# Performance work log

Measured on AMD Instinct MI355X. Metric: run time of the kernel, lower is better.

## Reference

```python
import jax, jax.numpy as jnp
import numpy as np

N = 200_000       # nodes
K = 16            # fixed in-degree
E = N * K         # edges
G = 4_000         # graphs (50 nodes each)
F_IN, H1, H2, OUT = 25, 16, 8, 2
EPS = 1e-5        # PyG std aggregator epsilon


def setup_inputs() -> dict:
    key = jax.random.key(0)
    ks = jax.random.split(key, 10)
    x = jax.random.normal(ks[0], (N, F_IN), jnp.float32)
    src = jax.random.randint(ks[1], (E,), 0, N)
    dst = jnp.repeat(jnp.arange(N), K)          # every node gets K incoming edges
    edge_index = jnp.stack([src, dst]).astype(jnp.int32)
    batch = jnp.repeat(jnp.arange(G), N // G).astype(jnp.int32)

    def lin(k, o, i):
        s = 1.0 / np.sqrt(i)
        kw, kb = jax.random.split(k)
        return (jax.random.uniform(kw, (o, i), jnp.float32, -s, s),
                jax.random.uniform(kb, (o,), jnp.float32, -s, s))

    w1_pre, b1_pre = lin(ks[2], F_IN, 2 * F_IN)
    w1_post, b1_post = lin(ks[3], H1, 12 * F_IN)
    w1_lin, b1_lin = lin(ks[4], H1, H1)
    w2_pre, b2_pre = lin(ks[5], H1, 2 * H1)
    w2_post, b2_post = lin(ks[6], H2, 12 * H1)
    w2_lin, b2_lin = lin(ks[7], H2, H2)
    fc_w, fc_b = lin(ks[8], OUT, H2)
    return dict(x=x, edge_index=edge_index, batch=batch,
                w1_pre=w1_pre, b1_pre=b1_pre, w1_post=w1_post, b1_post=b1_post,
                w1_lin=w1_lin, b1_lin=b1_lin,
                w2_pre=w2_pre, b2_pre=b2_pre, w2_post=w2_post, b2_post=b2_post,
                w2_lin=w2_lin, b2_lin=b2_lin, fc_w=fc_w, fc_b=fc_b)


def pna_conv(x, edge_index, wp, bp, wo, bo, wl, bl):
    src, dst = edge_index[0], edge_index[1]
    # message: pre-MLP on concat([x_i, x_j])  (x_i = target, x_j = source)
    m = jnp.concatenate([x[dst], x[src]], axis=-1) @ wp.T + bp  # [E, F]
    cnt = jax.ops.segment_sum(jnp.ones((m.shape[0],), m.dtype), dst, N)  # in-degree
    cnt_c = jnp.maximum(cnt, 1.0)[:, None]
    mean = jax.ops.segment_sum(m, dst, N) / cnt_c
    mean2 = jax.ops.segment_sum(m * m, dst, N) / cnt_c
    std = jnp.sqrt(jax.nn.relu(mean2 - mean * mean) + EPS)
    has = cnt[:, None] > 0
    mn = jnp.where(has, jax.ops.segment_min(m, dst, N), 0.0)
    mx = jnp.where(has, jax.ops.segment_max(m, dst, N), 0.0)
    agg = jnp.concatenate([mean, mn, mx, std], axis=-1)  # [N, 4F]
    # degree scalers (identity / amplification / attenuation)
    logd = jnp.log(jnp.maximum(cnt, 1.0) + 1.0)[:, None]
    avg_log = jnp.mean(jnp.log(cnt + 1.0))
    out = jnp.concatenate([agg, agg * (logd / avg_log), agg * (avg_log / logd)], axis=-1)
    out = out @ wo.T + bo   # post MLP
    return out @ wl.T + bl  # final lin


def reference(x, edge_index, batch,
              w1_pre, b1_pre, w1_post, b1_post, w1_lin, b1_lin,
              w2_pre, b2_pre, w2_post, b2_post, w2_lin, b2_lin,
              fc_w, fc_b):
    h = jax.nn.relu(pna_conv(x, edge_index, w1_pre, b1_pre, w1_post, b1_post, w1_lin, b1_lin))
    # dropout is identity in eval mode
    h = jax.nn.relu(pna_conv(h, edge_index, w2_pre, b2_pre, w2_post, b2_post, w2_lin, b2_lin))
    pooled = jax.ops.segment_sum(h, batch, G)  # global_add_pool -> [G, H2]
    logits = pooled @ fc_w.T + fc_b
    return jax.nn.log_softmax(logits, axis=1)
```

## Files before the change

### kernel.cpp

```cpp
#include <hip/hip_runtime.h>
#include <math.h>

#define N_NODES 200000
#define K_DEG 16
#define G_GRAPHS 4000
#define F_IN 25
#define EPSV 1e-5f

__device__ inline unsigned short f2bf(float f) {
    unsigned int u = __float_as_uint(f);
    u += 0x7fff + ((u >> 16) & 1);
    return (unsigned short)(u >> 16);
}
__device__ inline float bf2f(unsigned short h) {
    return __uint_as_float(((unsigned int)h) << 16);
}

__global__ void prep(const float* __restrict__ w1_pre, const float* __restrict__ b1_pre,
                     const float* __restrict__ w1_post, const float* __restrict__ b1_post,
                     const float* __restrict__ w1_lin, const float* __restrict__ b1_lin,
                     const float* __restrict__ w2_pre, const float* __restrict__ b2_pre,
                     const float* __restrict__ w2_post, const float* __restrict__ b2_post,
                     const float* __restrict__ w2_lin, const float* __restrict__ b2_lin,
                     float* __restrict__ C1ext, float* __restrict__ bvp1, float* __restrict__ P1,
                     float* __restrict__ C2p, float* __restrict__ bvp2, float* __restrict__ P2) {
    __shared__ float wp[4800];
    __shared__ float wl[256];
    __shared__ float mm[1600];
    __shared__ float aa[400];
    int tid = threadIdx.x;
    for (int i = tid; i < 4800; i += 256) wp[i] = w1_post[i];
    if (tid < 256) wl[tid] = w1_lin[tid];
    __syncthreads();
    for (int i = tid; i < 1600; i += 256) {
        int o = i / 100, j = i % 100;
        float s = 0.f;
        for (int h = 0; h < 16; ++h)
            s += wl[o * 16 + h] * (wp[h * 300 + j] + wp[h * 300 + 100 + j] + wp[h * 300 + 200 + j]);
        mm[i] = s;
    }
    __syncthreads();
    for (int i = tid; i < 400; i += 256) {
        int o = i / 25, f = i % 25;
        aa[i] = mm[o * 100 + f] + mm[o * 100 + 25 + f] + mm[o * 100 + 50 + f];
    }
    __syncthreads();
    for (int i = tid; i < 1728; i += 256) {
        int o = i / 108, c = i % 108;
        int st = c / 26, f = c % 26;
        C1ext[i] = (c < 104 && f < 25) ? mm[o * 100 + st * 25 + f] : 0.f;
    }
    for (int i = tid; i < 400; i += 256) {
        int o = i / 25, k = i % 25;
        float s = 0.f;
        for (int f = 0; f < 25; ++f) s += aa[o * 25 + f] * w1_pre[f * 50 + k];
        P1[i] = s;
    }
    if (tid < 16) {
        float s = b1_lin[tid];
        for (int h = 0; h < 16; ++h) s += wl[tid * 16 + h] * b1_post[h];
        for (int f = 0; f < 25; ++f) s += aa[tid * 25 + f] * b1_pre[f];
        bvp1[tid] = s;
    }
    __syncthreads();
    for (int i = tid; i < 1536; i += 256) wp[i] = w2_post[i];
    if (tid < 64) wl[tid] = w2_lin[tid];
    __syncthreads();
    for (int i = tid; i < 512; i += 256) {
        int o = i / 64, j = i % 64;
        float s = 0.f;
        for (int h = 0; h < 8; ++h)
            s += wl[o * 8 + h] * (wp[h * 192 + j] + wp[h * 192 + 64 + j] + wp[h * 192 + 128 + j]);
        mm[i] = s;
    }
    __syncthreads();
    if (tid < 128) {
        int o = tid / 16, f = tid % 16;
        aa[tid] = mm[o * 64 + f] + mm[o * 64 + 16 + f] + mm[o * 64 + 32 + f];
    }
    __syncthreads();
    for (int i = tid; i < 544; i += 256) {
        int o = i / 68, c = i % 68;
        C2p[i] = (c < 64) ? mm[o * 64 + c] : 0.f;
    }
    if (tid < 128) {
        int o = tid / 16, k = tid % 16;
        float s = 0.f;
        for (int f = 0; f < 16; ++f) s += aa[o * 16 + f] * w2_pre[f * 32 + k];
        P2[tid] = s;
    }
    if (tid < 8) {
        float s = b2_lin[tid];
        for (int h = 0; h < 8; ++h) s += wl[tid * 8 + h] * b2_post[h];
        for (int f = 0; f < 16; ++f) s += aa[tid * 16 + f] * b2_pre[f];
        bvp2[tid] = s;
    }
}

__global__ void __launch_bounds__(256) pre1(const float* __restrict__ x,
                                            const float* __restrict__ w1_pre,
                                            const float* __restrict__ P1,
                                            unsigned int* __restrict__ c1b_dw,
                                            float* __restrict__ d1) {
    __shared__ float xs[256 * 25];
    __shared__ float wls[25 * 25];
    __shared__ float pls[16 * 25];
    __shared__ unsigned int otile[256 * 17];
    int tid = threadIdx.x;
    int base = blockIdx.x * 256;
    for (int i = tid; i < 6400; i += 256) {
        int g = base * 25 + i;
        xs[i] = (g < N_NODES * F_IN) ? x[g] : 0.f;
    }
    for (int i = tid; i < 625; i += 256) {
        int f = i / 25, k = i % 25;
        wls[i] = w1_pre[f * 50 + 25 + k];
    }
    for (int i = tid; i < 400; i += 256) pls[i] = P1[i];
    __syncthreads();

    float xr[25];
#pragma unroll
    for (int k = 0; k < 25; ++k) xr[k] = xs[tid * 25 + k];

    unsigned int pk[16];
#pragma unroll
    for (int j = 0; j < 16; ++j) pk[j] = 0;
#pragma unroll
    for (int f = 0; f < 25; ++f) {
        float s = 0.f;
#pragma unroll
        for (int k = 0; k < 25; ++k) s += wls[f * 25 + k] * xr[k];
        unsigned int b = f2bf(s);
        pk[f >> 1] |= (f & 1) ? (b << 16) : b;
    }
#pragma unroll
    for (int j = 0; j < 16; ++j) otile[tid * 17 + j] = pk[j];
    __syncthreads();
    for (int i = tid; i < 4096; i += 256) {
        int g = base * 16 + i;
        if (g < N_NODES * 16) c1b_dw[g] = otile[(i >> 4) * 17 + (i & 15)];
    }
    __syncthreads();

    float* ftile = (float*)otile;
#pragma unroll
    for (int o = 0; o < 16; ++o) {
        float s = 0.f;
#pragma unroll
        for (int k = 0; k < 25; ++k) s += pls[o * 25 + k] * xr[k];
        ftile[tid * 17 + o] = s;
    }
    __syncthreads();
    for (int i = tid; i < 4096; i += 256) {
        int g = base * 16 + i;
        if (g < N_NODES * 16) d1[g] = ftile[(i >> 4) * 17 + (i & 15)];
    }
}

__global__ void __launch_bounds__(256) agg1(const unsigned int* __restrict__ c1u,
                                            const int* __restrict__ src,
                                            const float* __restrict__ d1,
                                            const float* __restrict__ C1ext,
                                            const float* __restrict__ bvp1,
                                            const float* __restrict__ w2_pre,
                                            const float* __restrict__ P2,
                                            unsigned short* __restrict__ c2b,
                                            float* __restrict__ d2) {
    __shared__ float cs[16 * 108];
    __shared__ float aggs[16 * 108];
    __shared__ float h1s[16 * 17];
    __shared__ float ws2[16 * 17];
    __shared__ float p2s[8 * 17];
    __shared__ float bvs[16];
    __shared__ int idxs[256];
    int tid = threadIdx.x;
    for (int i = tid; i < 1728; i += 256) cs[i] = C1ext[i];
    {
        int f = tid >> 4, k = tid & 15;
        ws2[f * 17 + k] = w2_pre[f * 32 + 16 + k];
    }
    if (tid < 128) p2s[(tid >> 4) * 17 + (tid & 15)] = P2[tid];
    if (tid < 16) bvs[tid] = bvp1[tid];
    idxs[tid] = src[blockIdx.x * 256 + tid];
    __syncthreads();

    int g = tid >> 4;
    int L = tid & 15;
    {
        int id[K_DEG];
#pragma unroll
        for (int e = 0; e < K_DEG; ++e) id[e] = idxs[g * 16 + e];
        unsigned int v[K_DEG];
#pragma unroll
        for (int e = 0; e < K_DEG; ++e) v[e] = c1u[id[e] * 16 + L];
        float s0 = 0.f, q0 = 0.f, n0 = 1e30f, x0 = -1e30f;
        float s1 = 0.f, q1 = 0.f, n1 = 1e30f, x1 = -1e30f;
#pragma unroll
        for (int e = 0; e < K_DEG; ++e) {
            float a = bf2f((unsigned short)(v[e] & 0xffff));
            float b = bf2f((unsigned short)(v[e] >> 16));
            s0 += a; q0 += a * a; n0 = fminf(n0, a); x0 = fmaxf(x0, a);
            s1 += b; q1 += b * b; n1 = fminf(n1, b); x1 = fmaxf(x1, b);
        }
        float me0 = s0 * (1.f / 16.f), me1 = s1 * (1.f / 16.f);
        float sd0 = sqrtf(fmaxf(q0 * (1.f / 16.f) - me0 * me0, 0.f) + EPSV);
        float sd1 = sqrtf(fmaxf(q1 * (1.f / 16.f) - me1 * me1, 0.f) + EPSV);
        if (L < 13) {
            float* r = aggs + g * 108 + 2 * L;
            *(float2*)(r)      = make_float2(me0, me1);
            *(float2*)(r + 26) = make_float2(n0, n1);
            *(float2*)(r + 52) = make_float2(x0, x1);
            *(float2*)(r + 78) = make_float2(sd0, sd1);
        } else if (L == 13) {
            *(float4*)(aggs + g * 108 + 104) = make_float4(0.f, 0.f, 0.f, 0.f);
        }
    }
    __syncthreads();

    {
        int nl = tid >> 4, o = tid & 15;
        int nn = blockIdx.x * 16 + nl;
        float s = bvs[o] + d1[nn * 16 + o];
        const float4* c4 = (const float4*)(cs + o * 108);
        const float4* a4 = (const float4*)(aggs + nl * 108);
#pragma unroll
        for (int j = 0; j < 27; ++j) {
            float4 cv = c4[j], av = a4[j];
            s += cv.x * av.x + cv.y * av.y + cv.z * av.z + cv.w * av.w;
        }
        h1s[nl * 17 + o] = fmaxf(s, 0.f);
    }
    __syncthreads();

    {
        int nl = tid >> 4, f = tid & 15;
        int nn = blockIdx.x * 16 + nl;
        const float* hr = h1s + nl * 17;
        float s = 0.f;
#pragma unroll
        for (int k = 0; k < 16; ++k) s += ws2[f * 17 + k] * hr[k];
        c2b[nn * 16 + f] = f2bf(s);
    }
    if (tid < 128) {
        int nl = tid >> 3, o = tid & 7;
        int nn = blockIdx.x * 16 + nl;
        const float* hr = h1s + nl * 17;
        float s = 0.f;
#pragma unroll
        for (int k = 0; k < 16; ++k) s += p2s[o * 17 + k] * hr[k];
        d2[nn * 8 + o] = s;
    }
}

__global__ void __launch_bounds__(256) agg2(const unsigned int* __restrict__ c2u,
                                            const int* __restrict__ src,
                                            const float* __restrict__ d2,
                                            const float* __restrict__ C2p,
                                            const float* __restrict__ bvp2,
                                            float* __restrict__ h2) {
    __shared__ float cs[8 * 68];
    __shared__ float ag[32 * 68];
    __shared__ float bvs[8];
    __shared__ int idxs[512];
    int tid = threadIdx.x;
    for (int i = tid; i < 544; i += 256) cs[i] = C2p[i];
    if (tid < 8) bvs[tid] = bvp2[tid];
    idxs[tid] = src[blockIdx.x * 512 + tid];
    idxs[tid + 256] = src[blockIdx.x * 512 + 256 + tid];
    __syncthreads();

    int g = tid >> 3;
    int L = tid & 7;
    {
        int id[K_DEG];
#pragma unroll
        for (int e = 0; e < K_DEG; ++e) id[e] = idxs[g * 16 + e];
        unsigned int v[K_DEG];
#pragma unroll
        for (int e = 0; e < K_DEG; ++e) v[e] = c2u[id[e] * 8 + L];
        float s0 = 0.f, q0 = 0.f, n0 = 1e30f, x0 = -1e30f;
        float s1 = 0.f, q1 = 0.f, n1 = 1e30f, x1 = -1e30f;
#pragma unroll
        for (int e = 0; e < K_DEG; ++e) {
            float a = bf2f((unsigned short)(v[e] & 0xffff));
            float b = bf2f((unsigned short)(v[e] >> 16));
            s0 += a; q0 += a * a; n0 = fminf(n0, a); x0 = fmaxf(x0, a);
            s1 += b; q1 += b * b; n1 = fminf(n1, b); x1 = fmaxf(x1, b);
        }
        float me0 = s0 * (1.f / 16.f), me1 = s1 * (1.f / 16.f);
        float sd0 = sqrtf(fmaxf(q0 * (1.f / 16.f) - me0 * me0, 0.f) + EPSV);
        float sd1 = sqrtf(fmaxf(q1 * (1.f / 16.f) - me1 * me1, 0.f) + EPSV);
        float* r = ag + g * 68 + 2 * L;
        *(float2*)(r)      = make_float2(me0, me1);
        *(float2*)(r + 16) = make_float2(n0, n1);
        *(float2*)(r + 32) = make_float2(x0, x1);
        *(float2*)(r + 48) = make_float2(sd0, sd1);
        if (L == 0) *(float4*)(ag + g * 68 + 64) = make_float4(0.f, 0.f, 0.f, 0.f);
    }
    __syncthreads();

    {
        int nl = tid >> 3, o = tid & 7;
        int nn = blockIdx.x * 32 + nl;
        float s = bvs[o] + d2[nn * 8 + o];
        const float4* c4 = (const float4*)(cs + o * 68);
        const float4* a4 = (const float4*)(ag + nl * 68);
#pragma unroll
        for (int j = 0; j < 17; ++j) {
            float4 cv = c4[j], av = a4[j];
            s += cv.x * av.x + cv.y * av.y + cv.z * av.z + cv.w * av.w;
        }
        h2[nn * 8 + o] = fmaxf(s, 0.f);
    }
}

__global__ void pool_fc(const float* __restrict__ h2, const float* __restrict__ fc_w,
                        const float* __restrict__ fc_b, float* __restrict__ out) {
    int wave = threadIdx.x >> 6;
    int lane = threadIdx.x & 63;
    int g = blockIdx.x * 4 + wave;
    float s0 = 0.f, s1 = 0.f;
    if (lane < 50) {
        const float* hr = h2 + (g * 50 + lane) * 8;
        float v[8];
#pragma unroll
        for (int o = 0; o < 8; ++o) v[o] = hr[o];
#pragma unroll
        for (int o = 0; o < 8; ++o) { s0 += fc_w[o] * v[o]; s1 += fc_w[8 + o] * v[o]; }
    }
#pragma unroll
    for (int off = 32; off > 0; off >>= 1) {
        s0 += __shfl_down(s0, off);
        s1 += __shfl_down(s1, off);
    }
    if (lane == 0) {
        float l0 = s0 + fc_b[0], l1 = s1 + fc_b[1];
        float m = fmaxf(l0, l1);
        float lse = m + logf(expf(l0 - m) + expf(l1 - m));
        out[g * 2]     = l0 - lse;
        out[g * 2 + 1] = l1 - lse;
    }
}

extern "C" void kernel_launch(void* const* d_in, const int* in_sizes, int n_in,
                              void* d_out, int out_size, void* d_ws, size_t ws_size,
                              hipStream_t stream) {
    const float* x       = (const float*)d_in[0];
    const int*   eidx    = (const int*)d_in[1];
    const float* w1_pre  = (const float*)d_in[3];
    const float* b1_pre  = (const float*)d_in[4];
    const float* w1_post = (const float*)d_in[5];
    const float* b1_post = (const float*)d_in[6];
    const float* w1_lin  = (const float*)d_in[7];
    const float* b1_lin  = (const float*)d_in[8];
    const float* w2_pre  = (const float*)d_in[9];
    const float* b2_pre  = (const float*)d_in[10];
    const float* w2_post = (const float*)d_in[11];
    const float* b2_post = (const float*)d_in[12];
    const float* w2_lin  = (const float*)d_in[13];
    const float* b2_lin  = (const float*)d_in[14];
    const float* fc_w    = (const float*)d_in[15];
    const float* fc_b    = (const float*)d_in[16];
    float* out = (float*)d_out;
    const int* src = eidx;

    char* ws = (char*)d_ws;
    unsigned int*   c1u = (unsigned int*)ws;
    unsigned short* c2b = (unsigned short*)(ws + 12800000);
    float* d1  = (float*)(ws + 19200000);
    float* d2  = (float*)(ws + 32000000);
    float* h2  = (float*)(ws + 38400000);
    float* C1ext = (float*)(ws + 44800000);
    float* bvp1  = C1ext + 1728;
    float* P1    = bvp1 + 16;
    float* C2p   = P1 + 400;
    float* bvp2  = C2p + 544;
    float* P2    = bvp2 + 8;

    prep<<<1, 256, 0, stream>>>(w1_pre, b1_pre, w1_post, b1_post, w1_lin, b1_lin,
                                w2_pre, b2_pre, w2_post, b2_post, w2_lin, b2_lin,
                                C1ext, bvp1, P1, C2p, bvp2, P2);
    pre1<<<(N_NODES + 255) / 256, 256, 0, stream>>>(x, w1_pre, P1, c1u, d1);
    agg1<<<N_NODES / 16, 256, 0, stream>>>(c1u, src, d1, C1ext, bvp1, w2_pre, P2, c2b, d2);
    agg2<<<N_NODES / 32, 256, 0, stream>>>((const unsigned int*)c2b, src, d2, C2p, bvp2, h2);
    pool_fc<<<G_GRAPHS / 4, 256, 0, stream>>>(h2, fc_w, fc_b, out);
}
```

Before: 241.9 us.

## Fold weight prep into consumer kernels and widen per-thread gather to 4 features

Removes the single-block prep kernel and has pre1, agg1 and agg2 each recompute their folded weight matrices and bias vectors in shared memory at block start. This drops one launch and a serial single-block step, but repeats the small weight-folding work in every block. The aggregation kernels now handle twice as many nodes per block, and each thread gathers uint2 (four bf16 features) per edge instead of one uint32. The goal is fewer, wider gather loads and better amortization of the per-block setup.

```diff
diff --git a/kernel.cpp b/kernel.cpp
--- a/kernel.cpp
+++ b/kernel.cpp
@@ -16,95 +16,18 @@
     return __uint_as_float(((unsigned int)h) << 16);
 }
 
-__global__ void prep(const float* __restrict__ w1_pre, const float* __restrict__ b1_pre,
-                     const float* __restrict__ w1_post, const float* __restrict__ b1_post,
-                     const float* __restrict__ w1_lin, const float* __restrict__ b1_lin,
-                     const float* __restrict__ w2_pre, const float* __restrict__ b2_pre,
-                     const float* __restrict__ w2_post, const float* __restrict__ b2_post,
-                     const float* __restrict__ w2_lin, const float* __restrict__ b2_lin,
-                     float* __restrict__ C1ext, float* __restrict__ bvp1, float* __restrict__ P1,
-                     float* __restrict__ C2p, float* __restrict__ bvp2, float* __restrict__ P2) {
-    __shared__ float wp[4800];
-    __shared__ float wl[256];
-    __shared__ float mm[1600];
-    __shared__ float aa[400];
-    int tid = threadIdx.x;
-    for (int i = tid; i < 4800; i += 256) wp[i] = w1_post[i];
-    if (tid < 256) wl[tid] = w1_lin[tid];
-    __syncthreads();
-    for (int i = tid; i < 1600; i += 256) {
-        int o = i / 100, j = i % 100;
-        float s = 0.f;
-        for (int h = 0; h < 16; ++h)
-            s += wl[o * 16 + h] * (wp[h * 300 + j] + wp[h * 300 + 100 + j] + wp[h * 300 + 200 + j]);
-        mm[i] = s;
-    }
-    __syncthreads();
-    for (int i = tid; i < 400; i += 256) {
-        int o = i / 25, f = i % 25;
-        aa[i] = mm[o * 100 + f] + mm[o * 100 + 25 + f] + mm[o * 100 + 50 + f];
-    }
-    __syncthreads();
-    for (int i = tid; i < 1728; i += 256) {
-        int o = i / 108, c = i % 108;
-        int st = c / 26, f = c % 26;
-        C1ext[i] = (c < 104 && f < 25) ? mm[o * 100 + st * 25 + f] : 0.f;
-    }
-    for (int i = tid; i < 400; i += 256) {
-        int o = i / 25, k = i % 25;
-        float s = 0.f;
-        for (int f = 0; f < 25; ++f) s += aa[o * 25 + f] * w1_pre[f * 50 + k];
-        P1[i] = s;
-    }
-    if (tid < 16) {
-        float s = b1_lin[tid];
-        for (int h = 0; h < 16; ++h) s += wl[tid * 16 + h] * b1_post[h];
-        for (int f = 0; f < 25; ++f) s += aa[tid * 25 + f] * b1_pre[f];
-        bvp1[tid] = s;
-    }
-    __syncthreads();
-    for (int i = tid; i < 1536; i += 256) wp[i] = w2_post[i];
-    if (tid < 64) wl[tid] = w2_lin[tid];
-    __syncthreads();
-    for (int i = tid; i < 512; i += 256) {
-        int o = i / 64, j = i % 64;
-        float s = 0.f;
-        for (int h = 0; h < 8; ++h)
-            s += wl[o * 8 + h] * (wp[h * 192 + j] + wp[h * 192 + 64 + j] + wp[h * 192 + 128 + j]);
-        mm[i] = s;
-    }
-    __syncthreads();
-    if (tid < 128) {
-        int o = tid / 16, f = tid % 16;
-        aa[tid] = mm[o * 64 + f] + mm[o * 64 + 16 + f] + mm[o * 64 + 32 + f];
-    }
-    __syncthreads();
-    for (int i = tid; i < 544; i += 256) {
-        int o = i / 68, c = i % 68;
-        C2p[i] = (c < 64) ? mm[o * 64 + c] : 0.f;
-    }
-    if (tid < 128) {
-        int o = tid / 16, k = tid % 16;
-        float s = 0.f;
-        for (int f = 0; f < 16; ++f) s += aa[o * 16 + f] * w2_pre[f * 32 + k];
-        P2[tid] = s;
-    }
-    if (tid < 8) {
-        float s = b2_lin[tid];
-        for (int h = 0; h < 8; ++h) s += wl[tid * 8 + h] * b2_post[h];
-        for (int f = 0; f < 16; ++f) s += aa[tid * 16 + f] * b2_pre[f];
-        bvp2[tid] = s;
-    }
-}
-
 __global__ void __launch_bounds__(256) pre1(const float* __restrict__ x,
                                             const float* __restrict__ w1_pre,
-                                            const float* __restrict__ P1,
+                                            const float* __restrict__ w1_post,
+                                            const float* __restrict__ w1_lin,
                                             unsigned int* __restrict__ c1b_dw,
                                             float* __restrict__ d1) {
     __shared__ float xs[256 * 25];
     __shared__ float wls[25 * 25];
     __shared__ float pls[16 * 25];
+    __shared__ float u1[16 * 25];
+    __shared__ float a1s[16 * 25];
+    __shared__ float wl[256];
     __shared__ unsigned int otile[256 * 17];
     int tid = threadIdx.x;
     int base = blockIdx.x * 256;
@@ -116,7 +39,29 @@
         int f = i / 25, k = i % 25;
         wls[i] = w1_pre[f * 50 + 25 + k];
     }
-    for (int i = tid; i < 400; i += 256) pls[i] = P1[i];
+    wl[tid] = w1_lin[tid];
+    for (int i = tid; i < 400; i += 256) {
+        int h = i / 25, f = i % 25;
+        const float* wp = w1_post + h * 300 + f;
+        u1[i] = wp[0] + wp[25] + wp[50] + wp[100] + wp[125] + wp[150] +
+                wp[200] + wp[225] + wp[250];
+    }
+    __syncthreads();
+    for (int i = tid; i < 400; i += 256) {
+        int o = i / 25, f = i % 25;
+        float s = 0.f;
+#pragma unroll
+        for (int h = 0; h < 16; ++h) s += wl[o * 16 + h] * u1[h * 25 + f];
+        a1s[i] = s;
+    }
+    __syncthreads();
+    for (int i = tid; i < 400; i += 256) {
+        int o = i / 25, k = i % 25;
+        float s = 0.f;
+#pragma unroll
+        for (int f = 0; f < 25; ++f) s += a1s[o * 25 + f] * w1_pre[f * 50 + k];
+        pls[i] = s;
+    }
     __syncthreads();
 
     float xr[25];
@@ -158,74 +103,149 @@
     }
 }
 
-__global__ void __launch_bounds__(256) agg1(const unsigned int* __restrict__ c1u,
+__global__ void __launch_bounds__(256) agg1(const uint2* __restrict__ c1u2,
                                             const int* __restrict__ src,
                                             const float* __restrict__ d1,
-                                            const float* __restrict__ C1ext,
-                                            const float* __restrict__ bvp1,
+                                            const float* __restrict__ w1_post,
+                                            const float* __restrict__ w1_lin,
+                                            const float* __restrict__ b1_post,
+                                            const float* __restrict__ b1_lin,
+                                            const float* __restrict__ b1_pre,
                                             const float* __restrict__ w2_pre,
-                                            const float* __restrict__ P2,
+                                            const float* __restrict__ w2_post,
+                                            const float* __restrict__ w2_lin,
                                             unsigned short* __restrict__ c2b,
                                             float* __restrict__ d2) {
-    __shared__ float cs[16 * 108];
-    __shared__ float aggs[16 * 108];
-    __shared__ float h1s[16 * 17];
+    __shared__ float cs[16 * 116];
+    __shared__ float aggs[32 * 116];
+    __shared__ float h1s[32 * 17];
     __shared__ float ws2[16 * 17];
     __shared__ float p2s[8 * 17];
     __shared__ float bvs[16];
-    __shared__ int idxs[256];
+    __shared__ float wl1[256];
+    __shared__ float wl2[64];
+    __shared__ int idxs[512];
     int tid = threadIdx.x;
-    for (int i = tid; i < 1728; i += 256) cs[i] = C1ext[i];
+    float* T1  = aggs;
+    float* T2  = aggs + 1600;
+    float* A1f = aggs + 2112;
+    float* A2f = aggs + 2512;
+
+    for (int i = tid; i < 1600; i += 256) {
+        int h = i / 100, j = i % 100;
+        const float* wp = w1_post + h * 300 + j;
+        T1[i] = wp[0] + wp[100] + wp[200];
+    }
+    for (int i = tid; i < 512; i += 256) {
+        int h = i >> 6, j = i & 63;
+        const float* wp = w2_post + h * 192 + j;
+        T2[i] = wp[0] + wp[64] + wp[128];
+    }
+    wl1[tid] = w1_lin[tid];
+    if (tid < 64) wl2[tid] = w2_lin[tid];
+    { int f = tid >> 4, k = tid & 15; ws2[f * 17 + k] = w2_pre[f * 32 + 16 + k]; }
+    __syncthreads();
+    for (int i = tid; i < 1792; i += 256) {
+        int o = i / 112, c = i % 112;
+        int st = c / 28, f = c % 28;
+        float s = 0.f;
+        if (f < 25) {
+            const float* tr = T1 + st * 25 + f;
+#pragma unroll
+            for (int h = 0; h < 16; ++h) s += wl1[o * 16 + h] * tr[h * 100];
+        }
+        cs[o * 116 + c] = s;
+    }
+    __syncthreads();
+    for (int i = tid; i < 400; i += 256) {
+        int o = i / 25, f = i % 25;
+        A1f[i] = cs[o * 116 + f] + cs[o * 116 + 28 + f] + cs[o * 116 + 56 + f];
+    }
+    if (tid < 128) {
+        int o = tid >> 4, f = tid & 15;
+        float s = 0.f;
+#pragma unroll
+        for (int h = 0; h < 8; ++h)
+            s += wl2[o * 8 + h] * (T2[h * 64 + f] + T2[h * 64 + 16 + f] + T2[h * 64 + 32 + f]);
+        A2f[tid] = s;
+    }
+    __syncthreads();
+    if (tid < 128) {
+        int o = tid >> 4, k = tid & 15;
+        float s = 0.f;
+#pragma unroll
+        for (int f = 0; f < 16; ++f) s += A2f[o * 16 + f] * w2_pre[f * 32 + k];
+        p2s[o * 17 + k] = s;
+    }
+    if (tid < 16) {
+        float s = b1_lin[tid];
+#pragma unroll
+        for (int h = 0; h < 16; ++h) s += wl1[tid * 16 + h] * b1_post[h];
+#pragma unroll
+        for (int f = 0; f < 25; ++f) s += A1f[tid * 25 + f] * b1_pre[f];
+        bvs[tid] = s;
+    }
+    idxs[tid] = src[blockIdx.x * 512 + tid];
+    idxs[256 + tid] = src[blockIdx.x * 512 + 256 + tid];
+    __syncthreads();
+
+    int g = tid >> 3, L = tid & 7;
+    float s0 = 0.f, s1 = 0.f, s2 = 0.f, s3 = 0.f;
+    float q0 = 0.f, q1 = 0.f, q2 = 0.f, q3 = 0.f;
+    float n0 = 1e30f, n1 = 1e30f, n2 = 1e30f, n3 = 1e30f;
+    float x0 = -1e30f, x1 = -1e30f, x2 = -1e30f, x3 = -1e30f;
+#pragma unroll
+    for (int b = 0; b < 2; ++b) {
+        int id[8];
+#pragma unroll
+        for (int e = 0; e < 8; ++e) id[e] = idxs[g * 16 + b * 8 + e];
+        uint2 v[8];
+#pragma unroll
+        for (int e = 0; e < 8; ++e) v[e] = c1u2[id[e] * 8 + L];
+#pragma unroll
+        for (int e = 0; e < 8; ++e) {
+            float a = bf2f((unsigned short)(v[e].x & 0xffff));
+            float bb = bf2f((unsigned short)(v[e].x >> 16));
+            float c = bf2f((unsigned short)(v[e].y & 0xffff));
+            float dd = bf2f((unsigned short)(v[e].y >> 16));
+            s0 += a;  q0 += a * a;   n0 = fminf(n0, a);  x0 = fmaxf(x0, a);
+            s1 += bb; q1 += bb * bb; n1 = fminf(n1, bb); x1 = fmaxf(x1, bb);
+            s2 += c;  q2 += c * c;   n2 = fminf(n2, c);  x2 = fmaxf(x2, c);
+            s3 += dd; q3 += dd * dd; n3 = fminf(n3, dd); x3 = fmaxf(x3, dd);
+        }
+    }
+    float me0 = s0 * (1.f / 16.f), me1 = s1 * (1.f / 16.f);
+    float me2 = s2 * (1.f / 16.f), me3 = s3 * (1.f / 16.f);
+    float sd0 = sqrtf(fmaxf(q0 * (1.f / 16.f) - me0 * me0, 0.f) + EPSV);
+    float sd1 = sqrtf(fmaxf(q1 * (1.f / 16.f) - me1 * me1, 0.f) + EPSV);
+    float sd2 = sqrtf(fmaxf(q2 * (1.f / 16.f) - me2 * me2, 0.f) + EPSV);
+    float sd3 = sqrtf(fmaxf(q3 * (1.f / 16.f) - me3 * me3, 0.f) + EPSV);
     {
-        int f = tid >> 4, k = tid & 15;
-        ws2[f * 17 + k] = w2_pre[f * 32 + 16 + k];
-    }
-    if (tid < 128) p2s[(tid >> 4) * 17 + (tid & 15)] = P2[tid];
-    if (tid < 16) bvs[tid] = bvp1[tid];
-    idxs[tid] = src[blockIdx.x * 256 + tid];
-    __syncthreads();
-
-    int g = tid >> 4;
-    int L = tid & 15;
-    {
-        int id[K_DEG];
-#pragma unroll
-        for (int e = 0; e < K_DEG; ++e) id[e] = idxs[g * 16 + e];
-        unsigned int v[K_DEG];
-#pragma unroll
-        for (int e = 0; e < K_DEG; ++e) v[e] = c1u[id[e] * 16 + L];
-        float s0 = 0.f, q0 = 0.f, n0 = 1e30f, x0 = -1e30f;
-        float s1 = 0.f, q1 = 0.f, n1 = 1e30f, x1 = -1e30f;
-#pragma unroll
-        for (int e = 0; e < K_DEG; ++e) {
-            float a = bf2f((unsigned short)(v[e] & 0xffff));
-            float b = bf2f((unsigned short)(v[e] >> 16));
-            s0 += a; q0 += a * a; n0 = fminf(n0, a); x0 = fmaxf(x0, a);
-            s1 += b; q1 += b * b; n1 = fminf(n1, b); x1 = fmaxf(x1, b);
-        }
-        float me0 = s0 * (1.f / 16.f), me1 = s1 * (1.f / 16.f);
-        float sd0 = sqrtf(fmaxf(q0 * (1.f / 16.f) - me0 * me0, 0.f) + EPSV);
-        float sd1 = sqrtf(fmaxf(q1 * (1.f / 16.f) - me1 * me1, 0.f) + EPSV);
-        if (L < 13) {
-            float* r = aggs + g * 108 + 2 * L;
-            *(float2*)(r)      = make_float2(me0, me1);
-            *(float2*)(r + 26) = make_float2(n0, n1);
-            *(float2*)(r + 52) = make_float2(x0, x1);
-            *(float2*)(r + 78) = make_float2(sd0, sd1);
-        } else if (L == 13) {
-            *(float4*)(aggs + g * 108 + 104) = make_float4(0.f, 0.f, 0.f, 0.f);
-        }
-    }
-    __syncthreads();
-
-    {
-        int nl = tid >> 4, o = tid & 15;
-        int nn = blockIdx.x * 16 + nl;
+        float* r = aggs + g * 116 + 4 * L;
+        if (L < 6) {
+            *(float4*)(r)      = make_float4(me0, me1, me2, me3);
+            *(float4*)(r + 28) = make_float4(n0, n1, n2, n3);
+            *(float4*)(r + 56) = make_float4(x0, x1, x2, x3);
+            *(float4*)(r + 84) = make_float4(sd0, sd1, sd2, sd3);
+        } else if (L == 6) {
+            *(float4*)(r)      = make_float4(me0, 0.f, 0.f, 0.f);
+            *(float4*)(r + 28) = make_float4(n0, 0.f, 0.f, 0.f);
+            *(float4*)(r + 56) = make_float4(x0, 0.f, 0.f, 0.f);
+            *(float4*)(r + 84) = make_float4(sd0, 0.f, 0.f, 0.f);
+        }
+    }
+    __syncthreads();
+
+#pragma unroll
+    for (int r2 = 0; r2 < 2; ++r2) {
+        int t2 = tid + 256 * r2;
+        int nl = t2 >> 4, o = t2 & 15;
+        int nn = blockIdx.x * 32 + nl;
         float s = bvs[o] + d1[nn * 16 + o];
-        const float4* c4 = (const float4*)(cs + o * 108);
-        const float4* a4 = (const float4*)(aggs + nl * 108);
-#pragma unroll
-        for (int j = 0; j < 27; ++j) {
+        const float4* c4 = (const float4*)(cs + o * 116);
+        const float4* a4 = (const float4*)(aggs + nl * 116);
+#pragma unroll
+        for (int j = 0; j < 28; ++j) {
             float4 cv = c4[j], av = a4[j];
             s += cv.x * av.x + cv.y * av.y + cv.z * av.z + cv.w * av.w;
         }
@@ -233,79 +253,131 @@
     }
     __syncthreads();
 
-    {
-        int nl = tid >> 4, f = tid & 15;
-        int nn = blockIdx.x * 16 + nl;
+#pragma unroll
+    for (int r2 = 0; r2 < 2; ++r2) {
+        int t2 = tid + 256 * r2;
+        int nl = t2 >> 4, f = t2 & 15;
+        int nn = blockIdx.x * 32 + nl;
         const float* hr = h1s + nl * 17;
         float s = 0.f;
 #pragma unroll
         for (int k = 0; k < 16; ++k) s += ws2[f * 17 + k] * hr[k];
         c2b[nn * 16 + f] = f2bf(s);
     }
-    if (tid < 128) {
-        int nl = tid >> 3, o = tid & 7;
-        int nn = blockIdx.x * 16 + nl;
-        const float* hr = h1s + nl * 17;
-        float s = 0.f;
-#pragma unroll
-        for (int k = 0; k < 16; ++k) s += p2s[o * 17 + k] * hr[k];
-        d2[nn * 8 + o] = s;
-    }
-}
-
-__global__ void __launch_bounds__(256) agg2(const unsigned int* __restrict__ c2u,
-                                            const int* __restrict__ src,
-                                            const float* __restrict__ d2,
-                                            const float* __restrict__ C2p,
-                                            const float* __restrict__ bvp2,
-                                            float* __restrict__ h2) {
-    __shared__ float cs[8 * 68];
-    __shared__ float ag[32 * 68];
-    __shared__ float bvs[8];
-    __shared__ int idxs[512];
-    int tid = threadIdx.x;
-    for (int i = tid; i < 544; i += 256) cs[i] = C2p[i];
-    if (tid < 8) bvs[tid] = bvp2[tid];
-    idxs[tid] = src[blockIdx.x * 512 + tid];
-    idxs[tid + 256] = src[blockIdx.x * 512 + 256 + tid];
-    __syncthreads();
-
-    int g = tid >> 3;
-    int L = tid & 7;
-    {
-        int id[K_DEG];
-#pragma unroll
-        for (int e = 0; e < K_DEG; ++e) id[e] = idxs[g * 16 + e];
-        unsigned int v[K_DEG];
-#pragma unroll
-        for (int e = 0; e < K_DEG; ++e) v[e] = c2u[id[e] * 8 + L];
-        float s0 = 0.f, q0 = 0.f, n0 = 1e30f, x0 = -1e30f;
-        float s1 = 0.f, q1 = 0.f, n1 = 1e30f, x1 = -1e30f;
-#pragma unroll
-        for (int e = 0; e < K_DEG; ++e) {
-            float a = bf2f((unsigned short)(v[e] & 0xffff));
-            float b = bf2f((unsigned short)(v[e] >> 16));
-            s0 += a; q0 += a * a; n0 = fminf(n0, a); x0 = fmaxf(x0, a);
-            s1 += b; q1 += b * b; n1 = fminf(n1, b); x1 = fmaxf(x1, b);
-        }
-        float me0 = s0 * (1.f / 16.f), me1 = s1 * (1.f / 16.f);
-        float sd0 = sqrtf(fmaxf(q0 * (1.f / 16.f) - me0 * me0, 0.f) + EPSV);
-        float sd1 = sqrtf(fmaxf(q1 * (1.f / 16.f) - me1 * me1, 0.f) + EPSV);
-        float* r = ag + g * 68 + 2 * L;
-        *(float2*)(r)      = make_float2(me0, me1);
-        *(float2*)(r + 16) = make_float2(n0, n1);
-        *(float2*)(r + 32) = make_float2(x0, x1);
-        *(float2*)(r + 48) = make_float2(sd0, sd1);
-        if (L == 0) *(float4*)(ag + g * 68 + 64) = make_float4(0.f, 0.f, 0.f, 0.f);
-    }
-    __syncthreads();
-
     {
         int nl = tid >> 3, o = tid & 7;
         int nn = blockIdx.x * 32 + nl;
-        float s = bvs[o] + d2[nn * 8 + o];
-        const float4* c4 = (const float4*)(cs + o * 68);
-        const float4* a4 = (const float4*)(ag + nl * 68);
+        const float* hr = h1s + nl * 17;
+        float s = 0.f;
+#pragma unroll
+        for (int k = 0; k < 16; ++k) s += p2s[o * 17 + k] * hr[k];
+        d2[nn * 8 + o] = s;
+    }
+}
+
+__global__ void __launch_bounds__(256) agg2(const uint2* __restrict__ c2u2,
+                                            const int* __restrict__ src,
+                                            const float* __restrict__ d2,
+                                            const float* __restrict__ w2_post,
+                                            const float* __restrict__ w2_lin,
+                                            const float* __restrict__ b2_post,
+                                            const float* __restrict__ b2_lin,
+                                            const float* __restrict__ b2_pre,
+                                            float* __restrict__ h2) {
+    __shared__ float cs2[8 * 68];
+    __shared__ float aggs2[64 * 68];
+    __shared__ float wl2[64];
+    __shared__ float bvs2[8];
+    __shared__ int idxs[1024];
+    int tid = threadIdx.x;
+    float* T2  = aggs2;
+    float* A2f = aggs2 + 512;
+
+    for (int i = tid; i < 512; i += 256) {
+        int h = i >> 6, j = i & 63;
+        const float* wp = w2_post + h * 192 + j;
+        T2[i] = wp[0] + wp[64] + wp[128];
+    }
+    if (tid < 64) wl2[tid] = w2_lin[tid];
+    __syncthreads();
+    for (int i = tid; i < 544; i += 256) {
+        int o = i / 68, c = i % 68;
+        float s = 0.f;
+        if (c < 64) {
+            const float* tr = T2 + c;
+#pragma unroll
+            for (int h = 0; h < 8; ++h) s += wl2[o * 8 + h] * tr[h * 64];
+        }
+        cs2[i] = s;
+    }
+    __syncthreads();
+    if (tid < 128) {
+        int o = tid >> 4, f = tid & 15;
+        A2f[tid] = cs2[o * 68 + f] + cs2[o * 68 + 16 + f] + cs2[o * 68 + 32 + f];
+    }
+    __syncthreads();
+    if (tid < 8) {
+        float s = b2_lin[tid];
+#pragma unroll
+        for (int h = 0; h < 8; ++h) s += wl2[tid * 8 + h] * b2_post[h];
+#pragma unroll
+        for (int f = 0; f < 16; ++f) s += A2f[tid * 16 + f] * b2_pre[f];
+        bvs2[tid] = s;
+    }
+#pragma unroll
+    for (int r2 = 0; r2 < 4; ++r2)
+        idxs[tid + 256 * r2] = src[blockIdx.x * 1024 + 256 * r2 + tid];
+    __syncthreads();
+
+    int g = tid >> 2, L = tid & 3;
+    float s0 = 0.f, s1 = 0.f, s2 = 0.f, s3 = 0.f;
+    float q0 = 0.f, q1 = 0.f, q2 = 0.f, q3 = 0.f;
+    float n0 = 1e30f, n1 = 1e30f, n2 = 1e30f, n3 = 1e30f;
+    float x0 = -1e30f, x1 = -1e30f, x2 = -1e30f, x3 = -1e30f;
+#pragma unroll
+    for (int b = 0; b < 2; ++b) {
+        int id[8];
+#pragma unroll
+        for (int e = 0; e < 8; ++e) id[e] = idxs[g * 16 + b * 8 + e];
+        uint2 v[8];
+#pragma unroll
+        for (int e = 0; e < 8; ++e) v[e] = c2u2[id[e] * 4 + L];
+#pragma unroll
+        for (int e = 0; e < 8; ++e) {
+            float a = bf2f((unsigned short)(v[e].x & 0xffff));
+            float bb = bf2f((unsigned short)(v[e].x >> 16));
+            float c = bf2f((unsigned short)(v[e].y & 0xffff));
+            float dd = bf2f((unsigned short)(v[e].y >> 16));
+            s0 += a;  q0 += a * a;   n0 = fminf(n0, a);  x0 = fmaxf(x0, a);
+            s1 += bb; q1 += bb * bb; n1 = fminf(n1, bb); x1 = fmaxf(x1, bb);
+            s2 += c;  q2 += c * c;   n2 = fminf(n2, c);  x2 = fmaxf(x2, c);
+            s3 += dd; q3 += dd * dd; n3 = fminf(n3, dd); x3 = fmaxf(x3, dd);
+        }
+    }
+    float me0 = s0 * (1.f / 16.f), me1 = s1 * (1.f / 16.f);
+    float me2 = s2 * (1.f / 16.f), me3 = s3 * (1.f / 16.f);
+    float sd0 = sqrtf(fmaxf(q0 * (1.f / 16.f) - me0 * me0, 0.f) + EPSV);
+    float sd1 = sqrtf(fmaxf(q1 * (1.f / 16.f) - me1 * me1, 0.f) + EPSV);
+    float sd2 = sqrtf(fmaxf(q2 * (1.f / 16.f) - me2 * me2, 0.f) + EPSV);
+    float sd3 = sqrtf(fmaxf(q3 * (1.f / 16.f) - me3 * me3, 0.f) + EPSV);
+    {
+        float* r = aggs2 + g * 68 + 4 * L;
+        *(float4*)(r)      = make_float4(me0, me1, me2, me3);
+        *(float4*)(r + 16) = make_float4(n0, n1, n2, n3);
+        *(float4*)(r + 32) = make_float4(x0, x1, x2, x3);
+        *(float4*)(r + 48) = make_float4(sd0, sd1, sd2, sd3);
+        if (L == 0) *(float4*)(aggs2 + g * 68 + 64) = make_float4(0.f, 0.f, 0.f, 0.f);
+    }
+    __syncthreads();
+
+#pragma unroll
+    for (int r2 = 0; r2 < 2; ++r2) {
+        int t2 = tid + 256 * r2;
+        int nl = t2 >> 3, o = t2 & 7;
+        int nn = blockIdx.x * 64 + nl;
+        float s = bvs2[o] + d2[nn * 8 + o];
+        const float4* c4 = (const float4*)(cs2 + o * 68);
+        const float4* a4 = (const float4*)(aggs2 + nl * 68);
 #pragma unroll
         for (int j = 0; j < 17; ++j) {
             float4 cv = c4[j], av = a4[j];
@@ -371,18 +443,12 @@
     float* d1  = (float*)(ws + 19200000);
     float* d2  = (float*)(ws + 32000000);
     float* h2  = (float*)(ws + 38400000);
-    float* C1ext = (float*)(ws + 44800000);
-    float* bvp1  = C1ext + 1728;
-    float* P1    = bvp1 + 16;
-    float* C2p   = P1 + 400;
-    float* bvp2  = C2p + 544;
-    float* P2    = bvp2 + 8;
-
-    prep<<<1, 256, 0, stream>>>(w1_pre, b1_pre, w1_post, b1_post, w1_lin, b1_lin,
-                                w2_pre, b2_pre, w2_post, b2_post, w2_lin, b2_lin,
-                                C1ext, bvp1, P1, C2p, bvp2, P2);
-    pre1<<<(N_NODES + 255) / 256, 256, 0, stream>>>(x, w1_pre, P1, c1u, d1);
-    agg1<<<N_NODES / 16, 256, 0, stream>>>(c1u, src, d1, C1ext, bvp1, w2_pre, P2, c2b, d2);
-    agg2<<<N_NODES / 32, 256, 0, stream>>>((const unsigned int*)c2b, src, d2, C2p, bvp2, h2);
+
+    pre1<<<(N_NODES + 255) / 256, 256, 0, stream>>>(x, w1_pre, w1_post, w1_lin, c1u, d1);
+    agg1<<<N_NODES / 32, 256, 0, stream>>>((const uint2*)c1u, src, d1,
+                                           w1_post, w1_lin, b1_post, b1_lin, b1_pre,
+                                           w2_pre, w2_post, w2_lin, c2b, d2);
+    agg2<<<N_NODES / 64, 256, 0, stream>>>((const uint2*)c2b, src, d2,
+                                           w2_post, w2_lin, b2_post, b2_lin, b2_pre, h2);
     pool_fc<<<G_GRAPHS / 4, 256, 0, stream>>>(h2, fc_w, fc_b, out);
 }
```

New measurement: 288.1 us. 1.19x slower.
